# Kernel optimization log

Hardware: AMD Instinct MI355X
Metric: run time of the kernel (lower is better)

Reference implementation:

```python
import jax, jax.numpy as jnp
import numpy as np

HID = 512
ROLES = 64

def setup_inputs() -> dict:
    key = jax.random.key(0)
    k1, k2, k3, k4, k5 = jax.random.split(key, 5)
    pred_input = jax.random.normal(k1, (8, 512, HID), dtype=jnp.float32)
    args_input = jax.random.normal(k2, (8, 512, HID), dtype=jnp.float32)
    # learned params (orthogonal init approximated by scaled normal for testing)
    U = jax.random.normal(k3, (HID, ROLES, HID), dtype=jnp.float32) * 0.02
    bias1 = jax.random.normal(k4, (1, HID * ROLES), dtype=jnp.float32) * 0.02
    bias2 = jax.random.normal(k5, (1, ROLES), dtype=jnp.float32) * 0.02
    return {"pred_input": pred_input, "args_input": args_input,
            "U": U, "bias1": bias1, "bias2": bias2}

def reference(pred_input, args_input, U, bias1, bias2):
    # dropout p=0.0 -> identity (eval behavior)
    b, t, h = pred_input.shape
    n = b * t
    pred = pred_input.reshape(n, h)          # [n, h]
    args = args_input.reshape(n, h)          # [n, h]
    # first = pred @ U.view(h, R*h) + bias1  -> [n, R*h]
    first = pred @ U.reshape(h, -1) + bias1
    # batched bilinear reduction: [n, R, h] x [n, h] -> [n, R]
    out = jnp.einsum('nrk,nk->nr', first.reshape(n, ROLES, h), args)
    return out + bias2
```

## Files before the change

### kernel.cpp

```cpp
#include <hip/hip_runtime.h>
#include <stdint.h>


#define HID   512
#define ROLES 64
#define NTOK  4096
#define BM    128
#define BN    128
#define BK    64

typedef __attribute__((ext_vector_type(8))) _Float16 f16x8;
typedef __attribute__((ext_vector_type(4))) _Float16 f16x4;
typedef __attribute__((ext_vector_type(4))) float    f32x4;

__device__ __forceinline__ void async16(const void* g, void* l) {
  __builtin_amdgcn_global_load_lds(
      (const __attribute__((address_space(1))) uint32_t*)g,
      (__attribute__((address_space(3))) uint32_t*)l, 16, 0, 0);
}

__global__ __launch_bounds__(256) void prep_fused(
    const float* __restrict__ pred_in, _Float16* __restrict__ predf,
    const float* __restrict__ U, _Float16* __restrict__ ut) {
  __shared__ float tile[128][65];
  const int bx = blockIdx.x;
  const int t  = threadIdx.x;

  if (bx >= 2048) {
    const int idx = (bx - 2048) * 256 + t;
    const float4 v = ((const float4*)pred_in)[idx];
    f16x4 o;
    o[0] = (_Float16)v.x; o[1] = (_Float16)v.y;
    o[2] = (_Float16)v.z; o[3] = (_Float16)v.w;
    ((f16x4*)predf)[idx] = o;
    return;
  }

  const int kb = bx & 7, hb = (bx >> 3) & 3, r = bx >> 5;
  const int h0 = hb * 128, k0 = kb * 64;
  const int rr = t >> 4, c4 = (t & 15) * 4;
#pragma unroll
  for (int pass = 0; pass < 8; pass++) {
    const int row = pass * 16 + rr;
    const float4 v = *(const float4*)(U + ((size_t)(h0 + row) * ROLES + r) * HID + k0 + c4);
    tile[row][c4 + 0] = v.x; tile[row][c4 + 1] = v.y;
    tile[row][c4 + 2] = v.z; tile[row][c4 + 3] = v.w;
  }
  __syncthreads();
  const int kr = t >> 4, hc = (t & 15) * 8;
#pragma unroll
  for (int pass = 0; pass < 4; pass++) {
    const int k = pass * 16 + kr;
    alignas(16) _Float16 hbuf[8];
#pragma unroll
    for (int j = 0; j < 8; j++) hbuf[j] = (_Float16)tile[hc + j][k];
    *(uint4*)(ut + ((size_t)r * HID + k0 + k) * HID + h0 + hc) = *(const uint4*)hbuf;
  }
}

__global__ __launch_bounds__(256, 3) void bilinear_mfma(
    const _Float16* __restrict__ predf, const _Float16* __restrict__ utf,
    const float* __restrict__ args, const float* __restrict__ bias1,
    float* __restrict__ part) {
  __shared__ _Float16 sA[BM * BK];
  __shared__ _Float16 sB[BN * BK];

  const int nblk = blockIdx.x, mblk = blockIdx.y, r = blockIdx.z;
  const int m0 = mblk * BM, n0 = nblk * BN;
  const int tid  = threadIdx.x;
  const int wave = tid >> 6, lane = tid & 63;
  const int col  = lane & 15, quad = lane >> 4;
  const int wm = (wave & 1) * 64, wn = (wave >> 1) * 64;

  const int i_loc = tid >> 3;
  const int ko    = ((tid & 7) ^ (i_loc & 7)) * 8;
  const size_t offA = (size_t)(m0 + i_loc) * HID + ko;
  const size_t offB = ((size_t)r * HID + n0 + i_loc) * HID + ko;
  const int ldsW = wave * 512;

  const int slotL8 = (quad ^ (col & 7)) * 8;
  const int slotH8 = slotL8 ^ 32;
  int rowA[4], rowB[4];
#pragma unroll
  for (int mt = 0; mt < 4; mt++) rowA[mt] = (wm + mt * 16 + col) * BK;
#pragma unroll
  for (int nt = 0; nt < 4; nt++) rowB[nt] = (wn + nt * 16 + col) * BK;

  f32x4 acc[4][4];
#pragma unroll
  for (int a = 0; a < 4; a++)
#pragma unroll
    for (int b = 0; b < 4; b++) acc[a][b] = (f32x4){0.f, 0.f, 0.f, 0.f};

  for (int k0 = 0; k0 < HID; k0 += BK) {
#pragma unroll
    for (int c = 0; c < 4; c++) {
      async16(predf + offA + (size_t)(c * 32) * HID + k0, sA + c * 2048 + ldsW);
      async16(utf   + offB + (size_t)(c * 32) * HID + k0, sB + c * 2048 + ldsW);
    }
    __syncthreads();

    {
      f16x8 a[4], b[4];
#pragma unroll
      for (int mt = 0; mt < 4; mt++) a[mt] = *(const f16x8*)(sA + rowA[mt] + slotL8);
#pragma unroll
      for (int nt = 0; nt < 4; nt++) b[nt] = *(const f16x8*)(sB + rowB[nt] + slotL8);
#pragma unroll
      for (int mt = 0; mt < 4; mt++)
#pragma unroll
        for (int nt = 0; nt < 4; nt++)
          acc[mt][nt] = __builtin_amdgcn_mfma_f32_16x16x32_f16(a[mt], b[nt], acc[mt][nt], 0, 0, 0);
    }
    {
      f16x8 a[4], b[4];
#pragma unroll
      for (int mt = 0; mt < 4; mt++) a[mt] = *(const f16x8*)(sA + rowA[mt] + slotH8);
#pragma unroll
      for (int nt = 0; nt < 4; nt++) b[nt] = *(const f16x8*)(sB + rowB[nt] + slotH8);
#pragma unroll
      for (int mt = 0; mt < 4; mt++)
#pragma unroll
        for (int nt = 0; nt < 4; nt++)
          acc[mt][nt] = __builtin_amdgcn_mfma_f32_16x16x32_f16(a[mt], b[nt], acc[mt][nt], 0, 0, 0);
    }
    __syncthreads();
  }

  float b1v[4];
#pragma unroll
  for (int nt = 0; nt < 4; nt++)
    b1v[nt] = bias1[r * HID + n0 + wn + nt * 16 + col];

  float sval[4][4];
#pragma unroll
  for (int mt = 0; mt < 4; mt++) {
#pragma unroll
    for (int reg = 0; reg < 4; reg++) {
      const int m = m0 + wm + mt * 16 + quad * 4 + reg;
      const float* arow = args + (size_t)m * HID + n0 + wn + col;
      float s = 0.f;
#pragma unroll
      for (int nt = 0; nt < 4; nt++)
        s += (acc[mt][nt][reg] + b1v[nt]) * arow[nt * 16];
      s += __shfl_xor(s, 1);
      s += __shfl_xor(s, 2);
      s += __shfl_xor(s, 4);
      s += __shfl_xor(s, 8);
      sval[mt][reg] = s;
    }
  }

  float* red = (float*)sA;
  if (wave >= 2 && col == 0) {
#pragma unroll
    for (int mt = 0; mt < 4; mt++)
#pragma unroll
      for (int reg = 0; reg < 4; reg++)
        red[wm + mt * 16 + quad * 4 + reg] = sval[mt][reg];
  }
  __syncthreads();
  if (wave < 2 && col == 0) {
    float* pbase = part + (((size_t)nblk * ROLES + r) << 12) + m0;
#pragma unroll
    for (int mt = 0; mt < 4; mt++) {
      const int row = wm + mt * 16 + quad * 4;
      float4 v;
      v.x = sval[mt][0] + red[row + 0];
      v.y = sval[mt][1] + red[row + 1];
      v.z = sval[mt][2] + red[row + 2];
      v.w = sval[mt][3] + red[row + 3];
      *(float4*)(pbase + row) = v;
    }
  }
}

__global__ __launch_bounds__(256) void reduce_k(const float* __restrict__ part,
                                                const float* __restrict__ b2,
                                                float* __restrict__ out) {
  const int idx = blockIdx.x * 256 + threadIdx.x;
  const int m = idx >> 6, r = idx & (ROLES - 1);
  float v = b2[r];
#pragma unroll
  for (int nb = 0; nb < 4; nb++)
    v += part[(((size_t)nb * ROLES + r) << 12) + m];
  out[idx] = v;
}

__global__ __launch_bounds__(256) void fallback_k(
    const float* __restrict__ pred, const float* __restrict__ args,
    const float* __restrict__ U, const float* __restrict__ b1,
    const float* __restrict__ b2, float* __restrict__ out) {
  const int idx = blockIdx.x * 256 + threadIdx.x;
  const int r = idx >> 12;
  const int n = idx & (NTOK - 1);
  const float* arow = args + (size_t)n * HID;
  const float* prow = pred + (size_t)n * HID;
  float acc = 0.f;
  for (int h = 0; h < HID; h++) {
    const float* urow = U + ((size_t)h * ROLES + r) * HID;
    float s = 0.f;
    for (int k = 0; k < HID; k++) s = fmaf(urow[k], arow[k], s);
    acc = fmaf(prow[h], s, acc);
  }
  float sb = 0.f;
  const float* brow = b1 + (size_t)r * HID;
  for (int k = 0; k < HID; k++) sb = fmaf(brow[k], arow[k], sb);
  out[(size_t)n * ROLES + r] = acc + sb + b2[r];
}

extern "C" void kernel_launch(void* const* d_in, const int* in_sizes, int n_in,
                              void* d_out, int out_size, void* d_ws, size_t ws_size,
                              hipStream_t stream) {
  const float* pred = (const float*)d_in[0];
  const float* args = (const float*)d_in[1];
  const float* U    = (const float*)d_in[2];
  const float* b1   = (const float*)d_in[3];
  const float* b2   = (const float*)d_in[4];
  float* out = (float*)d_out;

  const size_t PRED_ELEMS = (size_t)NTOK * HID;
  const size_t U_ELEMS    = (size_t)HID * ROLES * HID;
  const size_t PART_ELEMS = (size_t)4 * ROLES * NTOK;
  const size_t WS_NEEDED  = (PRED_ELEMS + U_ELEMS) * sizeof(_Float16)
                          + PART_ELEMS * sizeof(float);

  if (ws_size < WS_NEEDED) {
    hipLaunchKernelGGL(fallback_k, dim3((NTOK * ROLES) / 256), dim3(256), 0, stream,
                       pred, args, U, b1, b2, out);
    return;
  }

  _Float16* predf = (_Float16*)d_ws;
  _Float16* utf   = predf + PRED_ELEMS;
  float*    partb = (float*)(utf + U_ELEMS);

  hipLaunchKernelGGL(prep_fused, dim3(4096), dim3(256), 0, stream,
                     pred, predf, U, utf);
  hipLaunchKernelGGL(bilinear_mfma, dim3(HID / BN, NTOK / BM, ROLES), dim3(256), 0, stream,
                     predf, utf, args, b1, partb);
  hipLaunchKernelGGL(reduce_k, dim3((NTOK * ROLES) / 256), dim3(256), 0, stream,
                     partb, b2, out);
}
```

Measured before the change: 275.6 us.

## Double-buffer LDS tiles with BK=32 to overlap async loads with MFMA

The GEMM main loop now uses two LDS buffers with a K tile of 32. The next tile is fetched with global_load_lds while MFMAs run on the current one, which removes one barrier per step and hides load latency. The swizzle and load mapping are reworked for the narrower tile. In exchange there are twice as many loop iterations, each doing half the work, and whether the asynchronous LDS writes are correctly waited on before the barrier depends on the compiler inserting vmcnt waits.

```diff
diff --git a/kernel.cpp b/kernel.cpp
--- a/kernel.cpp
+++ b/kernel.cpp
@@ -7,7 +7,7 @@
 #define NTOK  4096
 #define BM    128
 #define BN    128
-#define BK    64
+#define BK    32
 
 typedef __attribute__((ext_vector_type(8))) _Float16 f16x8;
 typedef __attribute__((ext_vector_type(4))) _Float16 f16x4;
@@ -62,8 +62,8 @@
     const _Float16* __restrict__ predf, const _Float16* __restrict__ utf,
     const float* __restrict__ args, const float* __restrict__ bias1,
     float* __restrict__ part) {
-  __shared__ _Float16 sA[BM * BK];
-  __shared__ _Float16 sB[BN * BK];
+  __shared__ _Float16 sA[2][BM * BK];
+  __shared__ _Float16 sB[2][BN * BK];
 
   const int nblk = blockIdx.x, mblk = blockIdx.y, r = blockIdx.z;
   const int m0 = mblk * BM, n0 = nblk * BN;
@@ -72,19 +72,19 @@
   const int col  = lane & 15, quad = lane >> 4;
   const int wm = (wave & 1) * 64, wn = (wave >> 1) * 64;
 
-  const int i_loc = tid >> 3;
-  const int ko    = ((tid & 7) ^ (i_loc & 7)) * 8;
-  const size_t offA = (size_t)(m0 + i_loc) * HID + ko;
-  const size_t offB = ((size_t)r * HID + n0 + i_loc) * HID + ko;
-  const int ldsW = wave * 512;
-
-  const int slotL8 = (quad ^ (col & 7)) * 8;
-  const int slotH8 = slotL8 ^ 32;
+  const int i4 = tid >> 2;
+  const int s4 = tid & 3;
+  const int gch = s4 ^ ((i4 >> 1) & 3);
+  const size_t offA = (size_t)(m0 + i4) * HID + gch * 8;
+  const size_t offB = ((size_t)r * HID + n0 + i4) * HID + gch * 8;
+  const int ldsOff = tid * 8;
+
+  const int slot8 = (quad ^ ((col >> 1) & 3)) * 8;
   int rowA[4], rowB[4];
 #pragma unroll
-  for (int mt = 0; mt < 4; mt++) rowA[mt] = (wm + mt * 16 + col) * BK;
-#pragma unroll
-  for (int nt = 0; nt < 4; nt++) rowB[nt] = (wn + nt * 16 + col) * BK;
+  for (int mt = 0; mt < 4; mt++) rowA[mt] = (wm + mt * 16 + col) * BK + slot8;
+#pragma unroll
+  for (int nt = 0; nt < 4; nt++) rowB[nt] = (wn + nt * 16 + col) * BK + slot8;
 
   f32x4 acc[4][4];
 #pragma unroll
@@ -92,32 +92,28 @@
 #pragma unroll
     for (int b = 0; b < 4; b++) acc[a][b] = (f32x4){0.f, 0.f, 0.f, 0.f};
 
-  for (int k0 = 0; k0 < HID; k0 += BK) {
-#pragma unroll
-    for (int c = 0; c < 4; c++) {
-      async16(predf + offA + (size_t)(c * 32) * HID + k0, sA + c * 2048 + ldsW);
-      async16(utf   + offB + (size_t)(c * 32) * HID + k0, sB + c * 2048 + ldsW);
-    }
-    __syncthreads();
+  const _Float16* curA = sA[0]; _Float16* nxtA = sA[1];
+  const _Float16* curB = sB[0]; _Float16* nxtB = sB[1];
+
+  async16(predf + offA,                  (void*)(sA[0] + ldsOff));
+  async16(predf + offA + (size_t)64 * HID, (void*)(sA[0] + 2048 + ldsOff));
+  async16(utf   + offB,                  (void*)(sB[0] + ldsOff));
+  async16(utf   + offB + (size_t)64 * HID, (void*)(sB[0] + 2048 + ldsOff));
+  __syncthreads();
+
+  for (int t = 0; t < 15; t++) {
+    const int k1 = (t + 1) * BK;
+    async16(predf + offA + k1,                    (void*)(nxtA + ldsOff));
+    async16(predf + offA + (size_t)64 * HID + k1, (void*)(nxtA + 2048 + ldsOff));
+    async16(utf   + offB + k1,                    (void*)(nxtB + ldsOff));
+    async16(utf   + offB + (size_t)64 * HID + k1, (void*)(nxtB + 2048 + ldsOff));
 
     {
       f16x8 a[4], b[4];
 #pragma unroll
-      for (int mt = 0; mt < 4; mt++) a[mt] = *(const f16x8*)(sA + rowA[mt] + slotL8);
-#pragma unroll
-      for (int nt = 0; nt < 4; nt++) b[nt] = *(const f16x8*)(sB + rowB[nt] + slotL8);
-#pragma unroll
-      for (int mt = 0; mt < 4; mt++)
-#pragma unroll
-        for (int nt = 0; nt < 4; nt++)
-          acc[mt][nt] = __builtin_amdgcn_mfma_f32_16x16x32_f16(a[mt], b[nt], acc[mt][nt], 0, 0, 0);
-    }
-    {
-      f16x8 a[4], b[4];
-#pragma unroll
-      for (int mt = 0; mt < 4; mt++) a[mt] = *(const f16x8*)(sA + rowA[mt] + slotH8);
-#pragma unroll
-      for (int nt = 0; nt < 4; nt++) b[nt] = *(const f16x8*)(sB + rowB[nt] + slotH8);
+      for (int mt = 0; mt < 4; mt++) a[mt] = *(const f16x8*)(curA + rowA[mt]);
+#pragma unroll
+      for (int nt = 0; nt < 4; nt++) b[nt] = *(const f16x8*)(curB + rowB[nt]);
 #pragma unroll
       for (int mt = 0; mt < 4; mt++)
 #pragma unroll
@@ -125,6 +121,20 @@
           acc[mt][nt] = __builtin_amdgcn_mfma_f32_16x16x32_f16(a[mt], b[nt], acc[mt][nt], 0, 0, 0);
     }
     __syncthreads();
+    const _Float16* tA = curA; curA = nxtA; nxtA = (_Float16*)tA;
+    const _Float16* tB = curB; curB = nxtB; nxtB = (_Float16*)tB;
+  }
+  {
+    f16x8 a[4], b[4];
+#pragma unroll
+    for (int mt = 0; mt < 4; mt++) a[mt] = *(const f16x8*)(curA + rowA[mt]);
+#pragma unroll
+    for (int nt = 0; nt < 4; nt++) b[nt] = *(const f16x8*)(curB + rowB[nt]);
+#pragma unroll
+    for (int mt = 0; mt < 4; mt++)
+#pragma unroll
+      for (int nt = 0; nt < 4; nt++)
+        acc[mt][nt] = __builtin_amdgcn_mfma_f32_16x16x32_f16(a[mt], b[nt], acc[mt][nt], 0, 0, 0);
   }
 
   float b1v[4];
@@ -151,7 +161,7 @@
     }
   }
 
-  float* red = (float*)sA;
+  float* red = (float*)sA[0];
   if (wave >= 2 && col == 0) {
 #pragma unroll
     for (int mt = 0; mt < 4; mt++)
```

New measurement: 297.9 us. +8.1%, slower.

## Use 256x256 tiles with 8 waves and double-buffered async LDS pipeline

Applied to the files above, without the earlier changes.

Enlarges the GEMM tile to 256x256 with 512 threads (8 waves, each 128x64) and double-buffers the LDS stages so global-to-LDS loads for the next K step overlap the MFMA work. The inner loop is split into four sub-phases with barriers, s_setprio and sched_barrier to interleave LDS reads and MFMAs. The epilogue reduction now covers 4 column-waves, and the partial buffer is halved because there are only 2 N-blocks. This targets redundant global traffic and the load/compute serialization, at the cost of 128KB of LDS per block, higher register pressure and fewer resident blocks.

```diff
diff --git a/kernel.cpp b/kernel.cpp
--- a/kernel.cpp
+++ b/kernel.cpp
@@ -5,8 +5,8 @@
 #define HID   512
 #define ROLES 64
 #define NTOK  4096
-#define BM    128
-#define BN    128
+#define BM    256
+#define BN    256
 #define BK    64
 
 typedef __attribute__((ext_vector_type(8))) _Float16 f16x8;
@@ -58,73 +58,144 @@
   }
 }
 
-__global__ __launch_bounds__(256, 3) void bilinear_mfma(
+__global__ __launch_bounds__(512, 2) void bilinear_mfma(
     const _Float16* __restrict__ predf, const _Float16* __restrict__ utf,
     const float* __restrict__ args, const float* __restrict__ bias1,
     float* __restrict__ part) {
-  __shared__ _Float16 sA[BM * BK];
-  __shared__ _Float16 sB[BN * BK];
+  __shared__ _Float16 lds[2][32768];
 
   const int nblk = blockIdx.x, mblk = blockIdx.y, r = blockIdx.z;
   const int m0 = mblk * BM, n0 = nblk * BN;
   const int tid  = threadIdx.x;
-  const int wave = tid >> 6, lane = tid & 63;
+  const int lane = tid & 63, wid = tid >> 6;
   const int col  = lane & 15, quad = lane >> 4;
-  const int wm = (wave & 1) * 64, wn = (wave >> 1) * 64;
+  const int wr = wid >> 2, wc = wid & 3;
+  const int wm = wr * 128, wn = wc * 64;
 
   const int i_loc = tid >> 3;
   const int ko    = ((tid & 7) ^ (i_loc & 7)) * 8;
   const size_t offA = (size_t)(m0 + i_loc) * HID + ko;
   const size_t offB = ((size_t)r * HID + n0 + i_loc) * HID + ko;
-  const int ldsW = wave * 512;
+  const int ldsOff = tid * 8;
 
   const int slotL8 = (quad ^ (col & 7)) * 8;
   const int slotH8 = slotL8 ^ 32;
-  int rowA[4], rowB[4];
-#pragma unroll
-  for (int mt = 0; mt < 4; mt++) rowA[mt] = (wm + mt * 16 + col) * BK;
+  int rowA[8], rowB[4];
+#pragma unroll
+  for (int mt = 0; mt < 8; mt++) rowA[mt] = (wm + mt * 16 + col) * BK;
 #pragma unroll
   for (int nt = 0; nt < 4; nt++) rowB[nt] = (wn + nt * 16 + col) * BK;
 
-  f32x4 acc[4][4];
-#pragma unroll
-  for (int a = 0; a < 4; a++)
+  f32x4 acc[8][4];
+#pragma unroll
+  for (int a = 0; a < 8; a++)
 #pragma unroll
     for (int b = 0; b < 4; b++) acc[a][b] = (f32x4){0.f, 0.f, 0.f, 0.f};
 
-  for (int k0 = 0; k0 < HID; k0 += BK) {
+  auto STAGE = [&](int t, int buf) {
+    _Float16* bA = &lds[buf][0];
+    _Float16* bB = &lds[buf][16384];
+    const size_t kof = (size_t)t * BK;
 #pragma unroll
     for (int c = 0; c < 4; c++) {
-      async16(predf + offA + (size_t)(c * 32) * HID + k0, sA + c * 2048 + ldsW);
-      async16(utf   + offB + (size_t)(c * 32) * HID + k0, sB + c * 2048 + ldsW);
-    }
-    __syncthreads();
-
-    {
-      f16x8 a[4], b[4];
-#pragma unroll
-      for (int mt = 0; mt < 4; mt++) a[mt] = *(const f16x8*)(sA + rowA[mt] + slotL8);
-#pragma unroll
-      for (int nt = 0; nt < 4; nt++) b[nt] = *(const f16x8*)(sB + rowB[nt] + slotL8);
-#pragma unroll
-      for (int mt = 0; mt < 4; mt++)
-#pragma unroll
-        for (int nt = 0; nt < 4; nt++)
-          acc[mt][nt] = __builtin_amdgcn_mfma_f32_16x16x32_f16(a[mt], b[nt], acc[mt][nt], 0, 0, 0);
-    }
-    {
-      f16x8 a[4], b[4];
-#pragma unroll
-      for (int mt = 0; mt < 4; mt++) a[mt] = *(const f16x8*)(sA + rowA[mt] + slotH8);
-#pragma unroll
-      for (int nt = 0; nt < 4; nt++) b[nt] = *(const f16x8*)(sB + rowB[nt] + slotH8);
-#pragma unroll
-      for (int mt = 0; mt < 4; mt++)
-#pragma unroll
-        for (int nt = 0; nt < 4; nt++)
-          acc[mt][nt] = __builtin_amdgcn_mfma_f32_16x16x32_f16(a[mt], b[nt], acc[mt][nt], 0, 0, 0);
-    }
-    __syncthreads();
+      async16(predf + offA + (size_t)(c * 64) * HID + kof, bA + c * 4096 + ldsOff);
+      async16(utf   + offB + (size_t)(c * 64) * HID + kof, bB + c * 4096 + ldsOff);
+    }
+  };
+
+  STAGE(0, 0);
+  STAGE(1, 1);
+  asm volatile("s_waitcnt vmcnt(8)" ::: "memory");
+  __builtin_amdgcn_s_barrier();
+  __builtin_amdgcn_sched_barrier(0);
+
+  for (int t = 0; t < 8; ++t) {
+    const _Float16* bA = &lds[t & 1][0];
+    const _Float16* bB = &lds[t & 1][16384];
+
+    f16x8 aL[4], aH[4], bL[2], bH[2], cL[2], cH[2];
+
+#pragma unroll
+    for (int mt = 0; mt < 4; mt++) {
+      aL[mt] = *(const f16x8*)(bA + rowA[mt] + slotL8);
+      aH[mt] = *(const f16x8*)(bA + rowA[mt] + slotH8);
+    }
+#pragma unroll
+    for (int nt = 0; nt < 2; nt++) {
+      bL[nt] = *(const f16x8*)(bB + rowB[nt] + slotL8);
+      bH[nt] = *(const f16x8*)(bB + rowB[nt] + slotH8);
+    }
+    __builtin_amdgcn_s_setprio(1);
+#pragma unroll
+    for (int mt = 0; mt < 4; mt++)
+#pragma unroll
+      for (int nt = 0; nt < 2; nt++) {
+        acc[mt][nt] = __builtin_amdgcn_mfma_f32_16x16x32_f16(aL[mt], bL[nt], acc[mt][nt], 0, 0, 0);
+        acc[mt][nt] = __builtin_amdgcn_mfma_f32_16x16x32_f16(aH[mt], bH[nt], acc[mt][nt], 0, 0, 0);
+      }
+    __builtin_amdgcn_s_setprio(0);
+    __builtin_amdgcn_s_barrier();
+    __builtin_amdgcn_sched_barrier(0);
+
+#pragma unroll
+    for (int nt = 0; nt < 2; nt++) {
+      cL[nt] = *(const f16x8*)(bB + rowB[nt + 2] + slotL8);
+      cH[nt] = *(const f16x8*)(bB + rowB[nt + 2] + slotH8);
+    }
+    __builtin_amdgcn_s_setprio(1);
+#pragma unroll
+    for (int mt = 0; mt < 4; mt++)
+#pragma unroll
+      for (int nt = 0; nt < 2; nt++) {
+        acc[mt][nt + 2] = __builtin_amdgcn_mfma_f32_16x16x32_f16(aL[mt], cL[nt], acc[mt][nt + 2], 0, 0, 0);
+        acc[mt][nt + 2] = __builtin_amdgcn_mfma_f32_16x16x32_f16(aH[mt], cH[nt], acc[mt][nt + 2], 0, 0, 0);
+      }
+    __builtin_amdgcn_s_setprio(0);
+    __builtin_amdgcn_s_barrier();
+    __builtin_amdgcn_sched_barrier(0);
+
+#pragma unroll
+    for (int mt = 0; mt < 4; mt++) {
+      aL[mt] = *(const f16x8*)(bA + rowA[mt + 4] + slotL8);
+      aH[mt] = *(const f16x8*)(bA + rowA[mt + 4] + slotH8);
+    }
+    __builtin_amdgcn_s_setprio(1);
+#pragma unroll
+    for (int mt = 0; mt < 4; mt++)
+#pragma unroll
+      for (int nt = 0; nt < 2; nt++) {
+        acc[mt + 4][nt + 2] = __builtin_amdgcn_mfma_f32_16x16x32_f16(aL[mt], cL[nt], acc[mt + 4][nt + 2], 0, 0, 0);
+        acc[mt + 4][nt + 2] = __builtin_amdgcn_mfma_f32_16x16x32_f16(aH[mt], cH[nt], acc[mt + 4][nt + 2], 0, 0, 0);
+      }
+    __builtin_amdgcn_s_setprio(0);
+    __builtin_amdgcn_s_barrier();
+    __builtin_amdgcn_sched_barrier(0);
+
+#pragma unroll
+    for (int nt = 0; nt < 2; nt++) {
+      bL[nt] = *(const f16x8*)(bB + rowB[nt] + slotL8);
+      bH[nt] = *(const f16x8*)(bB + rowB[nt] + slotH8);
+    }
+    __builtin_amdgcn_s_setprio(1);
+#pragma unroll
+    for (int mt = 0; mt < 4; mt++)
+#pragma unroll
+      for (int nt = 0; nt < 2; nt++) {
+        acc[mt + 4][nt] = __builtin_amdgcn_mfma_f32_16x16x32_f16(aL[mt], bL[nt], acc[mt + 4][nt], 0, 0, 0);
+        acc[mt + 4][nt] = __builtin_amdgcn_mfma_f32_16x16x32_f16(aH[mt], bH[nt], acc[mt + 4][nt], 0, 0, 0);
+      }
+    __builtin_amdgcn_s_setprio(0);
+    __builtin_amdgcn_s_barrier();
+    __builtin_amdgcn_sched_barrier(0);
+
+    if (t < 6) {
+      STAGE(t + 2, t & 1);
+      asm volatile("s_waitcnt vmcnt(8)" ::: "memory");
+    } else if (t == 6) {
+      asm volatile("s_waitcnt vmcnt(0)" ::: "memory");
+    }
+    __builtin_amdgcn_s_barrier();
+    __builtin_amdgcn_sched_barrier(0);
   }
 
   float b1v[4];
@@ -132,9 +203,9 @@
   for (int nt = 0; nt < 4; nt++)
     b1v[nt] = bias1[r * HID + n0 + wn + nt * 16 + col];
 
-  float sval[4][4];
-#pragma unroll
-  for (int mt = 0; mt < 4; mt++) {
+  float sval[8][4];
+#pragma unroll
+  for (int mt = 0; mt < 8; mt++) {
 #pragma unroll
     for (int reg = 0; reg < 4; reg++) {
       const int m = m0 + wm + mt * 16 + quad * 4 + reg;
@@ -151,25 +222,25 @@
     }
   }
 
-  float* red = (float*)sA;
-  if (wave >= 2 && col == 0) {
-#pragma unroll
-    for (int mt = 0; mt < 4; mt++)
+  float* red = (float*)&lds[0][0];
+  if (wc != 0 && col == 0) {
+#pragma unroll
+    for (int mt = 0; mt < 8; mt++)
 #pragma unroll
       for (int reg = 0; reg < 4; reg++)
-        red[wm + mt * 16 + quad * 4 + reg] = sval[mt][reg];
+        red[(wc - 1) * 256 + wm + mt * 16 + quad * 4 + reg] = sval[mt][reg];
   }
   __syncthreads();
-  if (wave < 2 && col == 0) {
+  if (wc == 0 && col == 0) {
     float* pbase = part + (((size_t)nblk * ROLES + r) << 12) + m0;
 #pragma unroll
-    for (int mt = 0; mt < 4; mt++) {
+    for (int mt = 0; mt < 8; mt++) {
       const int row = wm + mt * 16 + quad * 4;
       float4 v;
-      v.x = sval[mt][0] + red[row + 0];
-      v.y = sval[mt][1] + red[row + 1];
-      v.z = sval[mt][2] + red[row + 2];
-      v.w = sval[mt][3] + red[row + 3];
+      v.x = sval[mt][0] + red[row + 0] + red[256 + row + 0] + red[512 + row + 0];
+      v.y = sval[mt][1] + red[row + 1] + red[256 + row + 1] + red[512 + row + 1];
+      v.z = sval[mt][2] + red[row + 2] + red[256 + row + 2] + red[512 + row + 2];
+      v.w = sval[mt][3] + red[row + 3] + red[256 + row + 3] + red[512 + row + 3];
       *(float4*)(pbase + row) = v;
     }
   }
@@ -182,7 +253,7 @@
   const int m = idx >> 6, r = idx & (ROLES - 1);
   float v = b2[r];
 #pragma unroll
-  for (int nb = 0; nb < 4; nb++)
+  for (int nb = 0; nb < 2; nb++)
     v += part[(((size_t)nb * ROLES + r) << 12) + m];
   out[idx] = v;
 }
@@ -221,7 +292,7 @@
 
   const size_t PRED_ELEMS = (size_t)NTOK * HID;
   const size_t U_ELEMS    = (size_t)HID * ROLES * HID;
-  const size_t PART_ELEMS = (size_t)4 * ROLES * NTOK;
+  const size_t PART_ELEMS = (size_t)2 * ROLES * NTOK;
   const size_t WS_NEEDED  = (PRED_ELEMS + U_ELEMS) * sizeof(_Float16)
                           + PART_ELEMS * sizeof(float);
 
@@ -237,7 +308,7 @@
 
   hipLaunchKernelGGL(prep_fused, dim3(4096), dim3(256), 0, stream,
                      pred, predf, U, utf);
-  hipLaunchKernelGGL(bilinear_mfma, dim3(HID / BN, NTOK / BM, ROLES), dim3(256), 0, stream,
+  hipLaunchKernelGGL(bilinear_mfma, dim3(HID / BN, NTOK / BM, ROLES), dim3(512), 0, stream,
                      predf, utf, args, b1, partb);
   hipLaunchKernelGGL(reduce_k, dim3((NTOK * ROLES) / 256), dim3(256), 0, stream,
                      partb, b2, out);
```

New measurement: 267.1 us. -3.1%, faster.
